# Optimization experiments

Measured on AMD Instinct MI355X. Metric: run time of the kernel, lower is better.

## Reference

```python
import jax, jax.numpy as jnp
import numpy as np

N = 8192
D_IN = 128
D_HID = 256  # hard-coded nn.Linear(input_dim, 256) in the module
D_OUT = 64
BN_EPS = 1e-5
LEAKY_SLOPE = 0.01


def setup_inputs() -> dict:
    key = jax.random.key(0)
    k_h, k_a, k_wt, k_wo = jax.random.split(key, 4)
    H = jax.random.normal(k_h, (N, D_IN), dtype=jnp.float32)
    # Fixed adjacency passed to __init__; values in [0,1) so mask=ceil(A*1e-5) is {0,1}
    A = jax.random.uniform(k_a, (N, N), dtype=jnp.float32)
    bn_weight = jnp.ones((D_IN,), jnp.float32)
    bn_bias = jnp.zeros((D_IN,), jnp.float32)
    W_theta = jax.random.normal(k_wt, (D_IN, D_HID), jnp.float32) * np.float32(1.0 / np.sqrt(D_IN))
    b_theta = jnp.zeros((D_HID,), jnp.float32)
    W_out = jax.random.normal(k_wo, (D_IN, D_OUT), jnp.float32) * np.float32(1.0 / np.sqrt(D_IN))
    b_out = jnp.zeros((D_OUT,), jnp.float32)
    return {"H": H, "A": A, "bn_weight": bn_weight, "bn_bias": bn_bias,
            "W_theta": W_theta, "b_theta": b_theta, "W_out": W_out, "b_out": b_out}


def reference(H, A, bn_weight, bn_bias, W_theta, b_theta, W_out, b_out):
    # BatchNorm1d in training mode: biased batch statistics over the node dim
    mean = jnp.mean(H, axis=0)
    var = jnp.mean(jnp.square(H - mean), axis=0)
    Hn = (H - mean) * jax.lax.rsqrt(var + BN_EPS) * bn_weight + bn_bias  # [N, D_IN]

    Hx = Hn @ W_theta + b_theta  # [N, 256]
    mask = jnp.ceil(A * 1e-5)    # constant {0,1} mask from fixed adjacency

    # Dynamic adjacency: clamp(sigmoid(Hx Hx^T), min=0.1) * mask + I
    S = jnp.clip(jax.nn.sigmoid(Hx @ Hx.T), 0.1, None)  # [N, N]
    Ad = S * mask + jnp.eye(N, dtype=H.dtype)

    # D^{-1/2} A D^{-1/2} via broadcast scaling (same math as diag matmuls)
    d = jax.lax.rsqrt(jnp.sum(Ad, axis=1))  # D^{-0.5}, [N]
    A_hat = Ad * d[:, None] * d[None, :]

    out = A_hat @ (Hn @ W_out + b_out)       # [N, D_OUT]
    out = jnp.where(out >= 0, out, LEAKY_SLOPE * out)  # LeakyReLU(0.01)
    return out, A_hat
```

## Files before the change

kernel.cpp:

```cpp
#include <hip/hip_runtime.h>
#include <hip/hip_bf16.h>

#define N 8192
#define DIN 128
#define DHID 256
#define DOUT 64
#define LDP 72
#define VP 136

typedef __attribute__((ext_vector_type(8))) short short8;
typedef __attribute__((ext_vector_type(8))) unsigned short u16x8;
typedef __attribute__((ext_vector_type(4))) float f32x4;

typedef __attribute__((address_space(1))) const unsigned int GlbU32;
typedef __attribute__((address_space(3))) unsigned int LdsU32;

__device__ inline void gload16(const void* g, void* l) {
  __builtin_amdgcn_global_load_lds((GlbU32*)g, (LdsU32*)l, 16, 0, 0);
}

#define LGKM_BAR()                                            \
  do {                                                        \
    asm volatile("s_waitcnt lgkmcnt(0)" ::: "memory");        \
    __builtin_amdgcn_sched_barrier(0);                        \
    __builtin_amdgcn_s_barrier();                             \
    __builtin_amdgcn_sched_barrier(0);                        \
  } while (0)

__device__ inline unsigned short f2bf(float x) {
  unsigned u = __float_as_uint(x);
  u += 0x7FFF + ((u >> 16) & 1);
  return (unsigned short)(u >> 16);
}
__device__ inline float bf2f(unsigned short u) {
  return __uint_as_float(((unsigned)u) << 16);
}
__device__ inline float sig_clip(float x) {
  float s = 1.0f / (1.0f + __expf(-x));
  return fmaxf(s, 0.1f);
}

__global__ __launch_bounds__(256) void maskpack(const float* __restrict__ A,
                                                unsigned long long* __restrict__ Mb) {
  size_t i = (size_t)blockIdx.x * 256 + threadIdx.x;
  size_t step = (size_t)gridDim.x * 256;
  int l = threadIdx.x & 63;
  for (; i < (size_t)N * N / 4; i += step) {
    f32x4 a = *(const f32x4*)&A[i * 4];
    unsigned long long b0 = __ballot(a[0] > 0.f);
    unsigned long long b1 = __ballot(a[1] > 0.f);
    unsigned long long b2 = __ballot(a[2] > 0.f);
    unsigned long long b3 = __ballot(a[3] > 0.f);
    size_t g = (i - l) >> 6;
    if (l < 4) {
      unsigned long long bb = (l == 0) ? b0 : (l == 1) ? b1 : (l == 2) ? b2 : b3;
      Mb[g * 4 + l] = bb;
    }
  }
}

__global__ void bn_stats(const float* __restrict__ H, const float* __restrict__ bnw,
                         const float* __restrict__ bnb, float* __restrict__ scale,
                         float* __restrict__ shift) {
  int f = blockIdx.x;
  int t = threadIdx.x;
  float s = 0.f, sq = 0.f;
  for (int r = t; r < N; r += 256) {
    float v = H[(size_t)r * DIN + f];
    s += v; sq += v * v;
  }
  __shared__ float ss[256], s2[256];
  ss[t] = s; s2[t] = sq;
  __syncthreads();
  for (int o = 128; o > 0; o >>= 1) {
    if (t < o) { ss[t] += ss[t + o]; s2[t] += s2[t + o]; }
    __syncthreads();
  }
  if (t == 0) {
    float mean = ss[0] * (1.0f / N);
    float var = s2[0] * (1.0f / N) - mean * mean;
    float sc = rsqrtf(var + 1e-5f) * bnw[f];
    scale[f] = sc;
    shift[f] = bnb[f] - mean * sc;
  }
}

__global__ __launch_bounds__(256) void proj(const float* __restrict__ H,
                     const float* __restrict__ scale, const float* __restrict__ shift,
                     const float* __restrict__ Wt, const float* __restrict__ bt,
                     const float* __restrict__ Wo, const float* __restrict__ bo,
                     unsigned short* __restrict__ Hx, unsigned short* __restrict__ M2T) {
  __shared__ float hn[8][DIN];
  int i0 = blockIdx.x * 8;
  int t = threadIdx.x;
  #pragma unroll
  for (int rep = 0; rep < 4; ++rep) {
    int idx = rep * 256 + t;
    int r = idx >> 7, c = idx & 127;
    float h = H[(size_t)(i0 + r) * DIN + c];
    hn[r][c] = fmaf(h, scale[c], shift[c]);
  }
  __syncthreads();
  {
    int c = t;
    float acc[8];
    float b = bt[c];
    #pragma unroll
    for (int r = 0; r < 8; ++r) acc[r] = b;
    for (int k = 0; k < DIN; ++k) {
      float w = Wt[k * DHID + c];
      #pragma unroll
      for (int r = 0; r < 8; ++r) acc[r] = fmaf(hn[r][k], w, acc[r]);
    }
    #pragma unroll
    for (int r = 0; r < 8; ++r) Hx[(size_t)(i0 + r) * DHID + c] = f2bf(acc[r]);
  }
  if (t < DOUT) {
    int c = t;
    float acc[8];
    float b = bo[c];
    #pragma unroll
    for (int r = 0; r < 8; ++r) acc[r] = b;
    for (int k = 0; k < DIN; ++k) {
      float w = Wo[k * DOUT + c];
      #pragma unroll
      for (int r = 0; r < 8; ++r) acc[r] = fmaf(hn[r][k], w, acc[r]);
    }
    u16x8 v;
    #pragma unroll
    for (int r = 0; r < 8; ++r) v[r] = f2bf(acc[r]);
    *(u16x8*)&M2T[(size_t)c * N + i0] = v;
  }
}

__global__ __launch_bounds__(256) void smat(const unsigned short* __restrict__ Hx,
                     const unsigned long long* __restrict__ Mb,
                     float* __restrict__ rowsum,
                     unsigned short* __restrict__ Vout) {
  int jt = blockIdx.x, it = blockIdx.y;
  if (jt < it) return;
  __shared__ unsigned short lsh[17408];
  __shared__ unsigned mbt32[128][4];
  __shared__ unsigned mbtT[128][4];
  __shared__ float scs[4][128];
  unsigned short* la = lsh;
  unsigned short* lb = lsh + 8192;
  int i0 = it * 128, j0 = jt * 128;
  int t = threadIdx.x;
  int w = t >> 6, l = t & 63;
  int lr = l & 15, lg = l >> 4;
  const bool offdiag = (it != jt);

  if (t < 128) {
    const unsigned long long* src = &Mb[(size_t)(i0 + t) * (N / 64) + (j0 >> 8) * 4];
    int sh = (j0 & 128) ? 32 : 0;
    #pragma unroll
    for (int e = 0; e < 4; ++e)
      mbt32[t][e] = (unsigned)(src[e] >> sh);
  }
  if (offdiag && t < 128) {
    const unsigned long long* srcT = &Mb[(size_t)(j0 + t) * (N / 64) + (i0 >> 8) * 4];
    int shT = (i0 & 128) ? 32 : 0;
    #pragma unroll
    for (int e = 0; e < 4; ++e)
      mbtT[t][e] = (unsigned)(srcT[e] >> shT);
  }

  f32x4 acc[2][8];
  f32x4 zero = {0.f, 0.f, 0.f, 0.f};
  #pragma unroll
  for (int m = 0; m < 2; ++m)
    #pragma unroll
    for (int n = 0; n < 8; ++n) acc[m][n] = zero;

  const int srow = l >> 3;
  const int scol = ((l & 7) ^ srow) * 8;
  const int fswz = (lr & 7) * 8;

  for (int c4 = 0; c4 < 4; ++c4) {
    int k0 = c4 * 64;
    __syncthreads();
    #pragma unroll
    for (int rp = 0; rp < 4; ++rp) {
      int chunk = rp * 4 + w;
      int row = chunk * 8 + srow;
      gload16(&Hx[(size_t)(i0 + row) * DHID + k0 + scol], &la[chunk * 512]);
      gload16(&Hx[(size_t)(j0 + row) * DHID + k0 + scol], &lb[chunk * 512]);
    }
    __syncthreads();
    #pragma unroll
    for (int kk = 0; kk < 2; ++kk) {
      int c = (kk * 32 + lg * 8) ^ fswz;
      short8 af[2], bf[8];
      #pragma unroll
      for (int m = 0; m < 2; ++m)
        af[m] = *(const short8*)&la[(w * 32 + m * 16 + lr) * 64 + c];
      #pragma unroll
      for (int n = 0; n < 8; ++n)
        bf[n] = *(const short8*)&lb[(n * 16 + lr) * 64 + c];
      #pragma unroll
      for (int m = 0; m < 2; ++m)
        #pragma unroll
        for (int n = 0; n < 8; ++n)
          acc[m][n] = __builtin_amdgcn_mfma_f32_16x16x32_bf16(af[m], bf[n], acc[m][n], 0, 0, 0);
    }
  }

  LGKM_BAR();

  #pragma unroll
  for (int m = 0; m < 2; ++m) {
    #pragma unroll
    for (int r = 0; r < 4; ++r) {
      int rl = w * 32 + m * 16 + lg * 4 + r;
      int gi = i0 + rl;
      unsigned mw = mbt32[rl][lr & 3];
      float part = 0.f;
      #pragma unroll
      for (int n = 0; n < 8; ++n) {
        int gj = j0 + n * 16 + lr;
        float s = sig_clip(acc[m][n][r]);
        acc[m][n][r] = s;
        float ms = ((mw >> (n * 4 + (lr >> 2))) & 1u) ? 1.f : 0.f;
        float v = s * ms + (gi == gj ? 1.f : 0.f);
        part += v;
        lsh[rl * VP + n * 16 + lr] = f2bf(v);
      }
      part += __shfl_xor(part, 1);
      part += __shfl_xor(part, 2);
      part += __shfl_xor(part, 4);
      part += __shfl_xor(part, 8);
      if (lr == 0) atomicAdd(&rowsum[gi], part);
    }
  }

  LGKM_BAR();
  #pragma unroll
  for (int pass = 0; pass < 8; ++pass) {
    int row = pass * 16 + (t >> 4);
    int cc = (t & 15) * 8;
    u16x8 vv = *(const u16x8*)&lsh[row * VP + cc];
    *(u16x8*)&Vout[(size_t)(i0 + row) * N + j0 + cc] = vv;
  }

  if (offdiag) {
    LGKM_BAR();
    float p[8];
    #pragma unroll
    for (int n = 0; n < 8; ++n) p[n] = 0.f;
    #pragma unroll
    for (int m = 0; m < 2; ++m) {
      #pragma unroll
      for (int r = 0; r < 4; ++r) {
        int rl = w * 32 + m * 16 + lg * 4 + r;
        int bitp = w * 8 + m * 4 + lg;
        #pragma unroll
        for (int n = 0; n < 8; ++n) {
          int c = n * 16 + lr;
          float ms = ((mbtT[c][r] >> bitp) & 1u) ? 1.f : 0.f;
          float v = acc[m][n][r] * ms;
          p[n] += v;
          lsh[c * VP + rl] = f2bf(v);
        }
      }
    }
    #pragma unroll
    for (int n = 0; n < 8; ++n) {
      p[n] += __shfl_xor(p[n], 16);
      p[n] += __shfl_xor(p[n], 32);
    }
    if (lg == 0) {
      #pragma unroll
      for (int n = 0; n < 8; ++n) scs[w][n * 16 + lr] = p[n];
    }
    LGKM_BAR();
    if (t < 128) {
      float cs = scs[0][t] + scs[1][t] + scs[2][t] + scs[3][t];
      atomicAdd(&rowsum[j0 + t], cs);
    }
    #pragma unroll
    for (int pass = 0; pass < 8; ++pass) {
      int row = pass * 16 + (t >> 4);
      int cc = (t & 15) * 8;
      u16x8 vv = *(const u16x8*)&lsh[row * VP + cc];
      *(u16x8*)&Vout[(size_t)(j0 + row) * N + i0 + cc] = vv;
    }
  }
}

__global__ void dfin(float* rs) {
  int i = blockIdx.x * 256 + threadIdx.x;
  if (i < N) rs[i] = rsqrtf(rs[i]);
}

__global__ __launch_bounds__(256) void outmm(const unsigned short* __restrict__ Vin,
                      const float* __restrict__ dd,
                      const unsigned short* __restrict__ M2T,
                      float* __restrict__ Ahat, float* __restrict__ out) {
  __shared__ unsigned short la[2][128 * LDP];
  int kc = blockIdx.x;
  int it = blockIdx.y;
  int i0 = it * 128;
  int jbase = kc * 512;
  int t = threadIdx.x;
  int w = t >> 6, l = t & 63;
  int lr = l & 15, lg = l >> 4;

  f32x4 acc[2][4];
  f32x4 zero = {0.f, 0.f, 0.f, 0.f};
  #pragma unroll
  for (int m = 0; m < 2; ++m)
    #pragma unroll
    for (int n = 0; n < 4; ++n) acc[m][n] = zero;

  const unsigned short* V = (const unsigned short*)Vin;
  const int row8 = t >> 3;
  const int cc8 = (t & 7) * 8;

  float di[4];
  #pragma unroll
  for (int rep = 0; rep < 4; ++rep) di[rep] = dd[i0 + rep * 32 + row8];

  u16x8 u[2][4];
  #pragma unroll
  for (int rep = 0; rep < 4; ++rep)
    u[0][rep] = *(const u16x8*)&V[(size_t)(i0 + rep * 32 + row8) * N + jbase + cc8];

  #pragma unroll
  for (int s = 0; s < 8; ++s) {
    const int cur = s & 1;
    const int j0 = jbase + s * 64;
    if (s < 7) {
      #pragma unroll
      for (int rep = 0; rep < 4; ++rep)
        u[cur ^ 1][rep] = *(const u16x8*)&V[(size_t)(i0 + rep * 32 + row8) * N + j0 + 64 + cc8];
    }
    short8 bfr[2][4];
    #pragma unroll
    for (int kk = 0; kk < 2; ++kk)
      #pragma unroll
      for (int n = 0; n < 4; ++n)
        bfr[kk][n] = *(const short8*)&M2T[(size_t)(n * 16 + lr) * N + j0 + kk * 32 + lg * 8];
    f32x4 dj0 = *(const f32x4*)&dd[j0 + cc8];
    f32x4 dj1 = *(const f32x4*)&dd[j0 + cc8 + 4];
    #pragma unroll
    for (int rep = 0; rep < 4; ++rep) {
      int row = rep * 32 + row8;
      size_t idx = (size_t)(i0 + row) * N + j0 + cc8;
      f32x4 s0, s1;
      s0[0] = bf2f(u[cur][rep][0]) * di[rep] * dj0[0];
      s0[1] = bf2f(u[cur][rep][1]) * di[rep] * dj0[1];
      s0[2] = bf2f(u[cur][rep][2]) * di[rep] * dj0[2];
      s0[3] = bf2f(u[cur][rep][3]) * di[rep] * dj0[3];
      s1[0] = bf2f(u[cur][rep][4]) * di[rep] * dj1[0];
      s1[1] = bf2f(u[cur][rep][5]) * di[rep] * dj1[1];
      s1[2] = bf2f(u[cur][rep][6]) * di[rep] * dj1[2];
      s1[3] = bf2f(u[cur][rep][7]) * di[rep] * dj1[3];
      *(f32x4*)&Ahat[idx] = s0;
      *(f32x4*)&Ahat[idx + 4] = s1;
      u16x8 b;
      b[0] = f2bf(s0[0]); b[1] = f2bf(s0[1]); b[2] = f2bf(s0[2]); b[3] = f2bf(s0[3]);
      b[4] = f2bf(s1[0]); b[5] = f2bf(s1[1]); b[6] = f2bf(s1[2]); b[7] = f2bf(s1[3]);
      *(u16x8*)&la[cur][row * LDP + cc8] = b;
    }
    LGKM_BAR();
    #pragma unroll
    for (int kk = 0; kk < 2; ++kk) {
      short8 af[2];
      #pragma unroll
      for (int m = 0; m < 2; ++m)
        af[m] = *(const short8*)&la[cur][(w * 32 + m * 16 + lr) * LDP + kk * 32 + lg * 8];
      #pragma unroll
      for (int m = 0; m < 2; ++m)
        #pragma unroll
        for (int n = 0; n < 4; ++n)
          acc[m][n] = __builtin_amdgcn_mfma_f32_16x16x32_bf16(af[m], bfr[kk][n], acc[m][n], 0, 0, 0);
    }
  }

  #pragma unroll
  for (int m = 0; m < 2; ++m)
    #pragma unroll
    for (int n = 0; n < 4; ++n)
      #pragma unroll
      for (int r = 0; r < 4; ++r) {
        int gi = i0 + w * 32 + m * 16 + lg * 4 + r;
        int gc = n * 16 + lr;
        atomicAdd(&out[(size_t)gi * DOUT + gc], acc[m][n][r]);
      }
}

__global__ void leaky(float* out) {
  int i = blockIdx.x * 256 + threadIdx.x;
  if (i < N * DOUT) {
    float x = out[i];
    out[i] = x >= 0.f ? x : 0.01f * x;
  }
}

extern "C" void kernel_launch(void* const* d_in, const int* in_sizes, int n_in,
                              void* d_out, int out_size, void* d_ws, size_t ws_size,
                              hipStream_t stream) {
  const float* H   = (const float*)d_in[0];
  const float* A   = (const float*)d_in[1];
  const float* bnw = (const float*)d_in[2];
  const float* bnb = (const float*)d_in[3];
  const float* Wt  = (const float*)d_in[4];
  const float* bt  = (const float*)d_in[5];
  const float* Wo  = (const float*)d_in[6];
  const float* bo  = (const float*)d_in[7];
  float* out = (float*)d_out;
  float* Ahat = out + (size_t)N * DOUT;

  char* ws = (char*)d_ws;
  float* scale  = (float*)(ws + 0);
  float* shift  = (float*)(ws + 512);
  float* rowsum = (float*)(ws + 4096);
  unsigned short* M2T = (unsigned short*)(ws + 65536);
  unsigned short* Hx  = (unsigned short*)(ws + 2097152);
  unsigned long long* Mb = (unsigned long long*)(ws + (size_t)(6u << 20));
  unsigned short* Vbf = (unsigned short*)(ws + (size_t)(14u << 20));

  hipMemsetAsync(rowsum, 0, N * sizeof(float), stream);
  hipMemsetAsync(out, 0, (size_t)N * DOUT * sizeof(float), stream);

  maskpack<<<4096, 256, 0, stream>>>(A, Mb);
  bn_stats<<<DIN, 256, 0, stream>>>(H, bnw, bnb, scale, shift);
  proj<<<N / 8, 256, 0, stream>>>(H, scale, shift, Wt, bt, Wo, bo, Hx, M2T);
  smat<<<dim3(64, 64), 256, 0, stream>>>(Hx, Mb, rowsum, Vbf);
  dfin<<<N / 256, 256, 0, stream>>>(rowsum);
  outmm<<<dim3(16, 64), 256, 0, stream>>>(Vbf, rowsum, M2T, Ahat, out);
  leaky<<<(N * DOUT + 255) / 256, 256, 0, stream>>>(out);
}
```

Before: 318.0 us.

## Fuse adjacency mask bit-packing into the similarity tile kernel

Removes the separate maskpack kernel and its packed-bitmask buffer. Each smat block now reads its own 128x128 tile of A (and the transposed tile for off-diagonal blocks) directly, spreading the loads across the four K-chunks so they overlap with the Hx tile loads, and builds the mask bits with wavefront ballots into shared memory. The bit layout changes to interleave even and odd columns, so the mask lookup indices are rewritten to match. This trades an extra kernel launch and a bitmask write/read round trip for more register use and ballot work inside the matmul kernel. A is still read in full (twice for off-diagonal tiles), and only half the grid does work.

Result: faster. 310.0 us (-2.5%).

```diff
diff --git a/kernel.cpp b/kernel.cpp
--- a/kernel.cpp
+++ b/kernel.cpp
@@ -11,6 +11,7 @@
 typedef __attribute__((ext_vector_type(8))) short short8;
 typedef __attribute__((ext_vector_type(8))) unsigned short u16x8;
 typedef __attribute__((ext_vector_type(4))) float f32x4;
+typedef __attribute__((ext_vector_type(2))) float f32x2;
 
 typedef __attribute__((address_space(1))) const unsigned int GlbU32;
 typedef __attribute__((address_space(3))) unsigned int LdsU32;
@@ -38,25 +39,6 @@
 __device__ inline float sig_clip(float x) {
   float s = 1.0f / (1.0f + __expf(-x));
   return fmaxf(s, 0.1f);
-}
-
-__global__ __launch_bounds__(256) void maskpack(const float* __restrict__ A,
-                                                unsigned long long* __restrict__ Mb) {
-  size_t i = (size_t)blockIdx.x * 256 + threadIdx.x;
-  size_t step = (size_t)gridDim.x * 256;
-  int l = threadIdx.x & 63;
-  for (; i < (size_t)N * N / 4; i += step) {
-    f32x4 a = *(const f32x4*)&A[i * 4];
-    unsigned long long b0 = __ballot(a[0] > 0.f);
-    unsigned long long b1 = __ballot(a[1] > 0.f);
-    unsigned long long b2 = __ballot(a[2] > 0.f);
-    unsigned long long b3 = __ballot(a[3] > 0.f);
-    size_t g = (i - l) >> 6;
-    if (l < 4) {
-      unsigned long long bb = (l == 0) ? b0 : (l == 1) ? b1 : (l == 2) ? b2 : b3;
-      Mb[g * 4 + l] = bb;
-    }
-  }
 }
 
 __global__ void bn_stats(const float* __restrict__ H, const float* __restrict__ bnw,
@@ -134,7 +116,7 @@
 }
 
 __global__ __launch_bounds__(256) void smat(const unsigned short* __restrict__ Hx,
-                     const unsigned long long* __restrict__ Mb,
+                     const float* __restrict__ A,
                      float* __restrict__ rowsum,
                      unsigned short* __restrict__ Vout) {
   int jt = blockIdx.x, it = blockIdx.y;
@@ -151,21 +133,6 @@
   int lr = l & 15, lg = l >> 4;
   const bool offdiag = (it != jt);
 
-  if (t < 128) {
-    const unsigned long long* src = &Mb[(size_t)(i0 + t) * (N / 64) + (j0 >> 8) * 4];
-    int sh = (j0 & 128) ? 32 : 0;
-    #pragma unroll
-    for (int e = 0; e < 4; ++e)
-      mbt32[t][e] = (unsigned)(src[e] >> sh);
-  }
-  if (offdiag && t < 128) {
-    const unsigned long long* srcT = &Mb[(size_t)(j0 + t) * (N / 64) + (i0 >> 8) * 4];
-    int shT = (i0 & 128) ? 32 : 0;
-    #pragma unroll
-    for (int e = 0; e < 4; ++e)
-      mbtT[t][e] = (unsigned)(srcT[e] >> shT);
-  }
-
   f32x4 acc[2][8];
   f32x4 zero = {0.f, 0.f, 0.f, 0.f};
   #pragma unroll
@@ -187,7 +154,41 @@
       gload16(&Hx[(size_t)(i0 + row) * DHID + k0 + scol], &la[chunk * 512]);
       gload16(&Hx[(size_t)(j0 + row) * DHID + k0 + scol], &lb[chunk * 512]);
     }
+    const int rbase = w * 32 + c4 * 8;
+    f32x2 au[8], al[8];
+    #pragma unroll
+    for (int rr = 0; rr < 8; ++rr)
+      au[rr] = *(const f32x2*)&A[(size_t)(i0 + rbase + rr) * N + j0 + 2 * l];
+    if (offdiag) {
+      #pragma unroll
+      for (int rr = 0; rr < 8; ++rr)
+        al[rr] = *(const f32x2*)&A[(size_t)(j0 + rbase + rr) * N + i0 + 2 * l];
+    }
     __syncthreads();
+    #pragma unroll
+    for (int rr = 0; rr < 8; ++rr) {
+      unsigned long long be = __ballot(au[rr][0] > 0.f);
+      unsigned long long bo = __ballot(au[rr][1] > 0.f);
+      if (l == 0) {
+        mbt32[rbase + rr][0] = (unsigned)be;
+        mbt32[rbase + rr][1] = (unsigned)(be >> 32);
+        mbt32[rbase + rr][2] = (unsigned)bo;
+        mbt32[rbase + rr][3] = (unsigned)(bo >> 32);
+      }
+    }
+    if (offdiag) {
+      #pragma unroll
+      for (int rr = 0; rr < 8; ++rr) {
+        unsigned long long be = __ballot(al[rr][0] > 0.f);
+        unsigned long long bo = __ballot(al[rr][1] > 0.f);
+        if (l == 0) {
+          mbtT[rbase + rr][0] = (unsigned)be;
+          mbtT[rbase + rr][1] = (unsigned)(be >> 32);
+          mbtT[rbase + rr][2] = (unsigned)bo;
+          mbtT[rbase + rr][3] = (unsigned)(bo >> 32);
+        }
+      }
+    }
     #pragma unroll
     for (int kk = 0; kk < 2; ++kk) {
       int c = (kk * 32 + lg * 8) ^ fswz;
@@ -214,14 +215,16 @@
     for (int r = 0; r < 4; ++r) {
       int rl = w * 32 + m * 16 + lg * 4 + r;
       int gi = i0 + rl;
-      unsigned mw = mbt32[rl][lr & 3];
+      unsigned w0 = mbt32[rl][(lr & 1) * 2];
+      unsigned w1 = mbt32[rl][(lr & 1) * 2 + 1];
       float part = 0.f;
       #pragma unroll
       for (int n = 0; n < 8; ++n) {
         int gj = j0 + n * 16 + lr;
         float s = sig_clip(acc[m][n][r]);
         acc[m][n][r] = s;
-        float ms = ((mw >> (n * 4 + (lr >> 2))) & 1u) ? 1.f : 0.f;
+        unsigned mwv = (n < 4) ? w0 : w1;
+        float ms = ((mwv >> ((n & 3) * 8 + (lr >> 1))) & 1u) ? 1.f : 0.f;
         float v = s * ms + (gi == gj ? 1.f : 0.f);
         part += v;
         lsh[rl * VP + n * 16 + lr] = f2bf(v);
@@ -253,11 +256,12 @@
       #pragma unroll
       for (int r = 0; r < 4; ++r) {
         int rl = w * 32 + m * 16 + lg * 4 + r;
-        int bitp = w * 8 + m * 4 + lg;
+        int wi = (r & 1) * 2 + (w >> 1);
+        int bitp = (w & 1) * 16 + m * 8 + lg * 2 + (r >> 1);
         #pragma unroll
         for (int n = 0; n < 8; ++n) {
           int c = n * 16 + lr;
-          float ms = ((mbtT[c][r] >> bitp) & 1u) ? 1.f : 0.f;
+          float ms = ((mbtT[c][wi] >> bitp) & 1u) ? 1.f : 0.f;
           float v = acc[m][n][r] * ms;
           p[n] += v;
           lsh[c * VP + rl] = f2bf(v);
@@ -418,16 +422,14 @@
   float* rowsum = (float*)(ws + 4096);
   unsigned short* M2T = (unsigned short*)(ws + 65536);
   unsigned short* Hx  = (unsigned short*)(ws + 2097152);
-  unsigned long long* Mb = (unsigned long long*)(ws + (size_t)(6u << 20));
   unsigned short* Vbf = (unsigned short*)(ws + (size_t)(14u << 20));
 
   hipMemsetAsync(rowsum, 0, N * sizeof(float), stream);
   hipMemsetAsync(out, 0, (size_t)N * DOUT * sizeof(float), stream);
 
-  maskpack<<<4096, 256, 0, stream>>>(A, Mb);
   bn_stats<<<DIN, 256, 0, stream>>>(H, bnw, bnb, scale, shift);
   proj<<<N / 8, 256, 0, stream>>>(H, scale, shift, Wt, bt, Wo, bo, Hx, M2T);
-  smat<<<dim3(64, 64), 256, 0, stream>>>(Hx, Mb, rowsum, Vbf);
+  smat<<<dim3(64, 64), 256, 0, stream>>>(Hx, A, rowsum, Vbf);
   dfin<<<N / 256, 256, 0, stream>>>(rowsum);
   outmm<<<dim3(16, 64), 256, 0, stream>>>(Vbf, rowsum, M2T, Ahat, out);
   leaky<<<(N * DOUT + 255) / 256, 256, 0, stream>>>(out);
```
